# Optimization experiments

Measured on AMD Instinct MI355X. Metric: run time of the kernel, lower is better.

Reference implementation:

```python
import jax, jax.numpy as jnp
import numpy as np

B, T1, T2, V, D, H = 1024, 256, 256, 32004, 50, 64


def _lstm_scan(x, h0, c0, Wih, Whh, b):
    """PyTorch-gate-order LSTM over time. x: [B,T,D]; returns hs, cs: [B,T,H]."""
    def step(carry, xt):
        h, c = carry
        g = xt @ Wih.T + h @ Whh.T + b  # [B, 4H], gate order i,f,g,o
        i, f, gg, o = jnp.split(g, 4, axis=-1)
        c = jax.nn.sigmoid(f) * c + jax.nn.sigmoid(i) * jnp.tanh(gg)
        h = jax.nn.sigmoid(o) * jnp.tanh(c)
        return (h, c), (h, c)
    _, (hs, cs) = jax.lax.scan(step, (h0, c0), jnp.swapaxes(x, 0, 1))
    return jnp.swapaxes(hs, 0, 1), jnp.swapaxes(cs, 0, 1)


def setup_inputs() -> dict:
    key = jax.random.key(0)
    ks = jax.random.split(key, 20)
    s = 1.0 / np.sqrt(H).astype(np.float32)
    inp = {
        "sentence1": jax.random.randint(ks[0], (B, T1), 0, V),
        "sentence2": jax.random.randint(ks[1], (B, T2), 0, V),
        "s1_len": jax.random.randint(ks[2], (B, 1, H), 0, T1),
        "s2_len": jax.random.randint(ks[3], (B, 1, H), 0, T2),
        "s1_s": jax.random.randint(ks[4], (B,), 0, 2),
        "s2_s": jax.random.randint(ks[5], (B,), 0, 2),
        "emb": jax.random.normal(ks[6], (V, D), jnp.float32),
        "Wih1": jax.random.uniform(ks[7], (4 * H, D), jnp.float32, -s, s),
        "Whh1": jax.random.uniform(ks[8], (4 * H, H), jnp.float32, -s, s),
        "bih1": jax.random.uniform(ks[9], (4 * H,), jnp.float32, -s, s),
        "bhh1": jax.random.uniform(ks[10], (4 * H,), jnp.float32, -s, s),
        "Wih2": jax.random.uniform(ks[11], (4 * H, D), jnp.float32, -s, s),
        "Whh2": jax.random.uniform(ks[12], (4 * H, H), jnp.float32, -s, s),
        "bih2": jax.random.uniform(ks[13], (4 * H,), jnp.float32, -s, s),
        "bhh2": jax.random.uniform(ks[14], (4 * H,), jnp.float32, -s, s),
        "Wl1": jax.random.uniform(ks[15], (128, H), jnp.float32, -s, s),
        "bl1": jax.random.uniform(ks[16], (128,), jnp.float32, -s, s),
        "Wl2": jax.random.uniform(ks[17], (4, 128), jnp.float32, -0.1, 0.1),
        "bl2": jax.random.uniform(ks[18], (4,), jnp.float32, -0.1, 0.1),
    }
    return inp


def reference(sentence1, sentence2, s1_len, s2_len, s1_s, s2_s, emb,
              Wih1, Whh1, bih1, bhh1, Wih2, Whh2, bih2, bhh2, Wl1, bl1, Wl2, bl2):
    embed1 = emb[sentence1]  # [B,T1,D]
    embed2 = emb[sentence2]  # [B,T2,D]
    h0 = jnp.zeros((B, H), embed1.dtype)
    c0 = jnp.zeros((B, H), embed1.dtype)
    # manual LSTMCell loop in original == scanned LSTM, keep all h,c per step
    h, c = _lstm_scan(embed1, h0, c0, Wih1, Whh1, bih1 + bhh1)  # [B,T1,H]
    gather_h = jnp.take_along_axis(h, s1_len, axis=1)[:, 0, :]  # [B,H]
    gather_c = jnp.take_along_axis(c, s1_len, axis=1)[:, 0, :]
    out, _ = _lstm_scan(embed2, gather_h, gather_c, Wih2, Whh2, bih2 + bhh2)
    out = jnp.take_along_axis(out, s2_len, axis=1)[:, 0, :]  # [B,H]
    out = jnp.tanh(out @ Wl1.T + bl1)  # dropout is identity at inference
    out = out @ Wl2.T + bl2  # [B,4]
    return out
```

## Files before the change

kernel.cpp:

```cpp
#include <hip/hip_runtime.h>

#define Bsz 1024
#define Tt  256
#define Vv  32004
#define Dd  50
#define Hh  64
#define MB  128

typedef __bf16 b16x8 __attribute__((ext_vector_type(8)));
typedef float  f32x4 __attribute__((ext_vector_type(4)));

__device__ __forceinline__ void barrier_novm() {
    asm volatile("s_waitcnt lgkmcnt(0)\n\ts_barrier" ::: "memory");
}
__device__ __forceinline__ float fexp2(float x) {
    float r;
    asm("v_exp_f32 %0, %1" : "=v"(r) : "v"(x));
    return r;
}
__device__ __forceinline__ float frcp(float x) {
    float r;
    asm("v_rcp_f32 %0, %1" : "=v"(r) : "v"(x));
    return r;
}
__device__ __forceinline__ float fsig(float x) {
    return frcp(1.0f + fexp2(x * -1.442695041f));
}
__device__ __forceinline__ float ftanh(float x) {
    return 2.0f * frcp(1.0f + fexp2(x * -2.885390082f)) - 1.0f;
}

__device__ __forceinline__ void cvt_hilo(const float* x, b16x8& hi, b16x8& lo) {
#pragma unroll
    for (int e = 0; e < 8; ++e) {
        const __bf16 h = (__bf16)x[e];
        hi[e] = h;
        lo[e] = (__bf16)(x[e] - (float)h);
    }
}

__launch_bounds__(256)
__global__ void build_tables(const float* __restrict__ emb,
                             const float* __restrict__ Wih1,
                             const float* __restrict__ bih1,
                             const float* __restrict__ bhh1,
                             const float* __restrict__ Wih2,
                             const float* __restrict__ bih2,
                             const float* __restrict__ bhh2,
                             float* __restrict__ tab1,
                             float* __restrict__ tab2) {
    const int tid  = threadIdx.x;
    const int w    = tid >> 6;
    const int lane = tid & 63;
    const int q    = lane >> 4;
    const int mn   = lane & 15;
    const int v0   = blockIdx.x * MB;

    const float* Wih = blockIdx.y ? Wih2 : Wih1;
    const float* bih = blockIdx.y ? bih2 : bih1;
    const float* bhh = blockIdx.y ? bhh2 : bhh1;
    float*       tab = blockIdx.y ? tab2 : tab1;

    __shared__ __align__(16) float wlds[256 * Dd];
    __shared__ __align__(16) float elds[MB * Dd];

    for (int d4 = tid; d4 < 256 * Dd / 4; d4 += 256)
        *(float4*)&wlds[4 * d4] = *(const float4*)(Wih + 4 * d4);
    {
        const int ebase = v0 * Dd;
        const int elim  = Vv * Dd - ebase;
        const int mx    = Vv * Dd - 1;
        for (int d4 = tid; d4 < MB * Dd / 4; d4 += 256) {
            const int d = 4 * d4;
            float4 v;
            if (d + 4 <= elim) {
                v = *(const float4*)(emb + ebase + d);
            } else {
                v.x = emb[min(ebase + d,     mx)];
                v.y = emb[min(ebase + d + 1, mx)];
                v.z = emb[min(ebase + d + 2, mx)];
                v.w = emb[min(ebase + d + 3, mx)];
            }
            *(float4*)&elds[d] = v;
        }
    }
    __syncthreads();

    b16x8 bh[4][2], bl[4][2];
    f32x4 bias4;
#pragma unroll
    for (int k = 0; k < 4; ++k) {
        const int g = 64 * k + 16 * w + mn;
        const int base = g * Dd;
        float x[8];
#pragma unroll
        for (int j = 0; j < 8; ++j) x[j] = wlds[base + 8 * q + j];
        cvt_hilo(x, bh[k][0], bl[k][0]);
#pragma unroll
        for (int j = 0; j < 8; ++j) {
            const int col = 32 + 8 * q + j;
            x[j] = (col < Dd) ? wlds[base + col] : 0.0f;
        }
        cvt_hilo(x, bh[k][1], bl[k][1]);
        bias4[k] = bih[g] + bhh[g];
    }

#pragma unroll 1
    for (int m = 0; m < MB / 16; ++m) {
        const int base = (16 * m + mn) * Dd;
        b16x8 ah[2], al[2];
        float x[8];
#pragma unroll
        for (int j = 0; j < 8; ++j) x[j] = elds[base + 8 * q + j];
        cvt_hilo(x, ah[0], al[0]);
#pragma unroll
        for (int j = 0; j < 8; ++j) {
            const int col = 32 + 8 * q + j;
            x[j] = (col < Dd) ? elds[base + col] : 0.0f;
        }
        cvt_hilo(x, ah[1], al[1]);

        f32x4 acc[4];
#pragma unroll
        for (int k = 0; k < 4; ++k) {
            f32x4 a = {0.0f, 0.0f, 0.0f, 0.0f};
#pragma unroll
            for (int kh = 0; kh < 2; ++kh) {
                a = __builtin_amdgcn_mfma_f32_16x16x32_bf16(ah[kh], bh[k][kh], a, 0, 0, 0);
                a = __builtin_amdgcn_mfma_f32_16x16x32_bf16(ah[kh], bl[k][kh], a, 0, 0, 0);
                a = __builtin_amdgcn_mfma_f32_16x16x32_bf16(al[kh], bh[k][kh], a, 0, 0, 0);
            }
            acc[k] = a;
        }
#pragma unroll
        for (int r = 0; r < 4; ++r) {
            const int vr = v0 + 16 * m + 4 * q + r;
            if (vr < Vv) {
                f32x4 o;
                o[0] = acc[0][r] + bias4[0];
                o[1] = acc[1][r] + bias4[1];
                o[2] = acc[2][r] + bias4[2];
                o[3] = acc[3][r] + bias4[3];
                *(f32x4*)(tab + (size_t)vr * 256 + (16 * w + mn) * 4) = o;
            }
        }
    }
}

__launch_bounds__(256, 1)
__global__ void lstm_main(const int*   __restrict__ s1,
                          const int*   __restrict__ s2,
                          const int*   __restrict__ len1,
                          const int*   __restrict__ len2,
                          const float* __restrict__ tab1,
                          const float* __restrict__ tab2,
                          const float* __restrict__ Whh1,
                          const float* __restrict__ Whh2,
                          const float* __restrict__ Wl1,
                          const float* __restrict__ bl1,
                          const float* __restrict__ Wl2,
                          const float* __restrict__ bl2,
                          float* __restrict__ out) {
    const int tid  = threadIdx.x;
    const int w    = tid >> 6;
    const int lane = tid & 63;
    const int q    = lane >> 4;
    const int mn   = lane & 15;
    const int row  = mn & 3;
    const bool sb0 = (mn >> 2) & 1;
    const bool sb1 = (mn >> 3) & 1;
    const int u_own = 16 * w + 4 * q + (mn >> 2);
    const int b0   = blockIdx.x * 4;

    __shared__ __align__(16) __bf16 hsh[2][4][96];
    __shared__ int   toklds[Tt][4];
    __shared__ float h2s[4][64];
    __shared__ float ys[4][128];

    float c = 0.0f, selh = 0.0f, selc = 0.0f;
    const f32x4 zero4 = {0.0f, 0.0f, 0.0f, 0.0f};

    for (int phase = 0; phase < 2; ++phase) {
        const float* tab  = phase ? tab2 : tab1;
        const float* Whh  = phase ? Whh2 : Whh1;
        const int*   sent = phase ? s2 : s1;
        const int*   lenp = phase ? len2 : len1;

        for (int i = tid; i < 4 * Tt; i += 256)
            toklds[i & 255][i >> 8] = sent[(size_t)(b0 + (i >> 8)) * Tt + (i & 255)];

        b16x8 af[8];
#pragma unroll
        for (int k = 0; k < 4; ++k) {
            const int gate = 64 * k + 16 * w + mn;
#pragma unroll
            for (int kh = 0; kh < 2; ++kh) {
                const float* ar = Whh + (size_t)gate * Hh + kh * 32 + q * 8;
                const float4 f0 = *(const float4*)ar;
                const float4 f1 = *(const float4*)(ar + 4);
                b16x8 a;
                a[0] = (__bf16)f0.x; a[1] = (__bf16)f0.y;
                a[2] = (__bf16)f0.z; a[3] = (__bf16)f0.w;
                a[4] = (__bf16)f1.x; a[5] = (__bf16)f1.y;
                a[6] = (__bf16)f1.z; a[7] = (__bf16)f1.w;
                af[2 * k + kh] = a;
            }
        }

        const int mi = lenp[(size_t)(b0 + row) * Hh + u_own];

        const float h0f = phase ? selh : 0.0f;
        c = phase ? selc : 0.0f;
        hsh[0][row][u_own] = (__bf16)h0f;
        selh = 0.0f; selc = 0.0f;
        __syncthreads();

        const float* tu = tab + 4 * u_own;
        f32x4 Sa, Sb, Sc, Sd;
        auto prime = [&](int t, f32x4& S) {
            S = *(const f32x4*)(tu + (size_t)toklds[t][row] * 256);
        };
        prime(0, Sa); prime(1, Sb); prime(2, Sc); prime(3, Sd);

        auto pick = [&](const f32x4& a) -> float {
            const float e01 = sb0 ? a[1] : a[0];
            const float e23 = sb0 ? a[3] : a[2];
            return sb1 ? e23 : e01;
        };

        auto step = [&](int t, f32x4& S, int rb, int wb) {
            const b16x8 bf0 = *(const b16x8*)&hsh[rb][row][q * 8];
            const b16x8 bf1 = *(const b16x8*)&hsh[rb][row][32 + q * 8];
            const int tnext = (t + 4 < Tt) ? t + 4 : Tt - 1;
            const int tk = toklds[tnext][row];

            f32x4 aG = __builtin_amdgcn_mfma_f32_16x16x32_bf16(af[4], bf0, zero4, 0, 0, 0);
            aG = __builtin_amdgcn_mfma_f32_16x16x32_bf16(af[5], bf1, aG, 0, 0, 0);
            f32x4 aI = __builtin_amdgcn_mfma_f32_16x16x32_bf16(af[0], bf0, zero4, 0, 0, 0);
            aI = __builtin_amdgcn_mfma_f32_16x16x32_bf16(af[1], bf1, aI, 0, 0, 0);
            f32x4 aF = __builtin_amdgcn_mfma_f32_16x16x32_bf16(af[2], bf0, zero4, 0, 0, 0);
            aF = __builtin_amdgcn_mfma_f32_16x16x32_bf16(af[3], bf1, aF, 0, 0, 0);
            f32x4 aO = __builtin_amdgcn_mfma_f32_16x16x32_bf16(af[6], bf0, zero4, 0, 0, 0);
            aO = __builtin_amdgcn_mfma_f32_16x16x32_bf16(af[7], bf1, aO, 0, 0, 0);

            const float gG = pick(aG) + S[2];
            const float gI = pick(aI) + S[0];
            const float gF = pick(aF) + S[1];
            const float gO = pick(aO) + S[3];
            S = *(const f32x4*)(tu + (size_t)tk * 256);

            const float gv = ftanh(gG);
            const float iv = fsig(gI);
            const float fv = fsig(gF);
            const float ov = fsig(gO);
            c = fv * c + iv * gv;
            const float hv = ov * ftanh(c);
            hsh[wb][row][u_own] = (__bf16)hv;
            if (t == mi) { selh = hv; selc = c; }
            barrier_novm();
        };

        for (int t = 0; t < Tt; t += 4) {
            step(t,     Sa, 0, 1);
            step(t + 1, Sb, 1, 0);
            step(t + 2, Sc, 0, 1);
            step(t + 3, Sd, 1, 0);
        }
    }

    h2s[row][u_own] = selh;
    __syncthreads();
#pragma unroll
    for (int p = 0; p < 2; ++p) {
        const int idx = tid + 256 * p;
        const int rr = idx >> 7, n = idx & 127;
        float a = bl1[n];
        const float* wl = Wl1 + n * 64;
#pragma unroll 8
        for (int k = 0; k < 64; ++k) a += h2s[rr][k] * wl[k];
        ys[rr][n] = ftanh(a);
    }
    __syncthreads();
    if (tid < 16) {
        const int rr = tid >> 2, o = tid & 3;
        float a = bl2[o];
        const float* wl = Wl2 + o * 128;
#pragma unroll 8
        for (int k = 0; k < 128; ++k) a += ys[rr][k] * wl[k];
        out[(size_t)(b0 + rr) * 4 + o] = a;
    }
}

extern "C" void kernel_launch(void* const* d_in, const int* in_sizes, int n_in,
                              void* d_out, int out_size, void* d_ws, size_t ws_size,
                              hipStream_t stream) {
    const int*   s1   = (const int*)d_in[0];
    const int*   s2   = (const int*)d_in[1];
    const int*   l1   = (const int*)d_in[2];
    const int*   l2   = (const int*)d_in[3];
    const float* emb  = (const float*)d_in[6];
    const float* Wih1 = (const float*)d_in[7];
    const float* Whh1 = (const float*)d_in[8];
    const float* bih1 = (const float*)d_in[9];
    const float* bhh1 = (const float*)d_in[10];
    const float* Wih2 = (const float*)d_in[11];
    const float* Whh2 = (const float*)d_in[12];
    const float* bih2 = (const float*)d_in[13];
    const float* bhh2 = (const float*)d_in[14];
    const float* Wl1  = (const float*)d_in[15];
    const float* bl1  = (const float*)d_in[16];
    const float* Wl2  = (const float*)d_in[17];
    const float* bl2  = (const float*)d_in[18];
    float* out = (float*)d_out;

    float* tab1 = (float*)d_ws;
    float* tab2 = tab1 + (size_t)Vv * 256;

    dim3 grid((Vv + MB - 1) / MB, 2);
    build_tables<<<grid, 256, 0, stream>>>(emb, Wih1, bih1, bhh1,
                                           Wih2, bih2, bhh2, tab1, tab2);
    lstm_main<<<Bsz / 4, 256, 0, stream>>>(s1, s2, l1, l2, tab1, tab2,
                                           Whh1, Whh2, Wl1, bl1, Wl2, bl2, out);
}
```

Before: 281.5 us.

## Process two batch-row groups per block and fold activation scales into weights

Each block now handles 8 batch rows, interleaving two independent LSTM recurrences per thread to hide MFMA and transcendental latency per serial step. Gate prescale constants for exp2-based sigmoid/tanh are folded into the precomputed input table and the recurrent weights, removing multiplies from the step. Tokens are stored row-major in LDS and fetched as int4 vectors with deeper table prefetch. The grid halves, leaving fewer blocks than CUs, and per-thread register pressure rises.

```diff
diff --git a/kernel.cpp b/kernel.cpp
--- a/kernel.cpp
+++ b/kernel.cpp
@@ -23,9 +23,8 @@
     asm("v_rcp_f32 %0, %1" : "=v"(r) : "v"(x));
     return r;
 }
-__device__ __forceinline__ float fsig(float x) {
-    return frcp(1.0f + fexp2(x * -1.442695041f));
-}
+__device__ __forceinline__ float fsig_p(float x)  { return frcp(1.0f + fexp2(x)); }
+__device__ __forceinline__ float ftanh_p(float x) { return 2.0f * frcp(1.0f + fexp2(x)) - 1.0f; }
 __device__ __forceinline__ float ftanh(float x) {
     return 2.0f * frcp(1.0f + fexp2(x * -2.885390082f)) - 1.0f;
 }
@@ -105,6 +104,8 @@
         bias4[k] = bih[g] + bhh[g];
     }
 
+    const f32x4 scale4 = {-1.442695041f, -1.442695041f, -2.885390082f, -1.442695041f};
+
 #pragma unroll 1
     for (int m = 0; m < MB / 16; ++m) {
         const int base = (16 * m + mn) * Dd;
@@ -137,10 +138,10 @@
             const int vr = v0 + 16 * m + 4 * q + r;
             if (vr < Vv) {
                 f32x4 o;
-                o[0] = acc[0][r] + bias4[0];
-                o[1] = acc[1][r] + bias4[1];
-                o[2] = acc[2][r] + bias4[2];
-                o[3] = acc[3][r] + bias4[3];
+                o[0] = (acc[0][r] + bias4[0]) * scale4[0];
+                o[1] = (acc[1][r] + bias4[1]) * scale4[1];
+                o[2] = (acc[2][r] + bias4[2]) * scale4[2];
+                o[3] = (acc[3][r] + bias4[3]) * scale4[3];
                 *(f32x4*)(tab + (size_t)vr * 256 + (16 * w + mn) * 4) = o;
             }
         }
@@ -166,18 +167,20 @@
     const int lane = tid & 63;
     const int q    = lane >> 4;
     const int mn   = lane & 15;
-    const int row  = mn & 3;
+    const int rowA = mn & 3;
+    const int rowB = rowA + 4;
     const bool sb0 = (mn >> 2) & 1;
     const bool sb1 = (mn >> 3) & 1;
     const int u_own = 16 * w + 4 * q + (mn >> 2);
-    const int b0   = blockIdx.x * 4;
-
-    __shared__ __align__(16) __bf16 hsh[2][4][96];
-    __shared__ int   toklds[Tt][4];
-    __shared__ float h2s[4][64];
-    __shared__ float ys[4][128];
-
-    float c = 0.0f, selh = 0.0f, selc = 0.0f;
+    const int b0   = blockIdx.x * 8;
+
+    __shared__ __align__(16) __bf16 hsh[2][8][96];
+    __shared__ __align__(16) int toklds[8][Tt + 8];
+    __shared__ float h2s[8][64];
+    __shared__ float ys[8][128];
+
+    float cA = 0.0f, selhA = 0.0f, selcA = 0.0f;
+    float cB = 0.0f, selhB = 0.0f, selcB = 0.0f;
     const f32x4 zero4 = {0.0f, 0.0f, 0.0f, 0.0f};
 
     for (int phase = 0; phase < 2; ++phase) {
@@ -186,41 +189,57 @@
         const int*   sent = phase ? s2 : s1;
         const int*   lenp = phase ? len2 : len1;
 
-        for (int i = tid; i < 4 * Tt; i += 256)
-            toklds[i & 255][i >> 8] = sent[(size_t)(b0 + (i >> 8)) * Tt + (i & 255)];
+        for (int i = tid; i < 8 * Tt; i += 256)
+            toklds[i >> 8][i & 255] = sent[(size_t)(b0 + (i >> 8)) * Tt + (i & 255)];
 
         b16x8 af[8];
 #pragma unroll
         for (int k = 0; k < 4; ++k) {
             const int gate = 64 * k + 16 * w + mn;
+            const float sck = (k == 2) ? -2.885390082f : -1.442695041f;
 #pragma unroll
             for (int kh = 0; kh < 2; ++kh) {
                 const float* ar = Whh + (size_t)gate * Hh + kh * 32 + q * 8;
                 const float4 f0 = *(const float4*)ar;
                 const float4 f1 = *(const float4*)(ar + 4);
                 b16x8 a;
-                a[0] = (__bf16)f0.x; a[1] = (__bf16)f0.y;
-                a[2] = (__bf16)f0.z; a[3] = (__bf16)f0.w;
-                a[4] = (__bf16)f1.x; a[5] = (__bf16)f1.y;
-                a[6] = (__bf16)f1.z; a[7] = (__bf16)f1.w;
+                a[0] = (__bf16)(f0.x * sck); a[1] = (__bf16)(f0.y * sck);
+                a[2] = (__bf16)(f0.z * sck); a[3] = (__bf16)(f0.w * sck);
+                a[4] = (__bf16)(f1.x * sck); a[5] = (__bf16)(f1.y * sck);
+                a[6] = (__bf16)(f1.z * sck); a[7] = (__bf16)(f1.w * sck);
                 af[2 * k + kh] = a;
             }
         }
 
-        const int mi = lenp[(size_t)(b0 + row) * Hh + u_own];
-
-        const float h0f = phase ? selh : 0.0f;
-        c = phase ? selc : 0.0f;
-        hsh[0][row][u_own] = (__bf16)h0f;
-        selh = 0.0f; selc = 0.0f;
+        const int miA = lenp[(size_t)(b0 + rowA) * Hh + u_own];
+        const int miB = lenp[(size_t)(b0 + rowB) * Hh + u_own];
+
+        hsh[0][rowA][u_own] = (__bf16)(phase ? selhA : 0.0f);
+        hsh[0][rowB][u_own] = (__bf16)(phase ? selhB : 0.0f);
+        cA = phase ? selcA : 0.0f;
+        cB = phase ? selcB : 0.0f;
+        selhA = 0.0f; selcA = 0.0f; selhB = 0.0f; selcB = 0.0f;
         __syncthreads();
 
         const float* tu = tab + 4 * u_own;
-        f32x4 Sa, Sb, Sc, Sd;
-        auto prime = [&](int t, f32x4& S) {
-            S = *(const f32x4*)(tu + (size_t)toklds[t][row] * 256);
-        };
-        prime(0, Sa); prime(1, Sb); prime(2, Sc); prime(3, Sd);
+
+        int4 a0c = *(const int4*)&toklds[rowA][0];
+        int4 aC1 = *(const int4*)&toklds[rowA][4];
+        int4 aC2 = *(const int4*)&toklds[rowA][8];
+        int4 b0c = *(const int4*)&toklds[rowB][0];
+        int4 bC1 = *(const int4*)&toklds[rowB][4];
+        int4 bC2 = *(const int4*)&toklds[rowB][8];
+
+        f32x4 SA0, SA1, SA2, SA3, SA4, SA5, SA6, SA7;
+        f32x4 SB0, SB1, SB2, SB3, SB4, SB5, SB6, SB7;
+        SA0 = *(const f32x4*)(tu + (size_t)a0c.x * 256);
+        SA1 = *(const f32x4*)(tu + (size_t)a0c.y * 256);
+        SA2 = *(const f32x4*)(tu + (size_t)a0c.z * 256);
+        SA3 = *(const f32x4*)(tu + (size_t)a0c.w * 256);
+        SB0 = *(const f32x4*)(tu + (size_t)b0c.x * 256);
+        SB1 = *(const f32x4*)(tu + (size_t)b0c.y * 256);
+        SB2 = *(const f32x4*)(tu + (size_t)b0c.z * 256);
+        SB3 = *(const f32x4*)(tu + (size_t)b0c.w * 256);
 
         auto pick = [&](const f32x4& a) -> float {
             const float e01 = sb0 ? a[1] : a[0];
@@ -228,60 +247,100 @@
             return sb1 ? e23 : e01;
         };
 
-        auto step = [&](int t, f32x4& S, int rb, int wb) {
-            const b16x8 bf0 = *(const b16x8*)&hsh[rb][row][q * 8];
-            const b16x8 bf1 = *(const b16x8*)&hsh[rb][row][32 + q * 8];
-            const int tnext = (t + 4 < Tt) ? t + 4 : Tt - 1;
-            const int tk = toklds[tnext][row];
-
-            f32x4 aG = __builtin_amdgcn_mfma_f32_16x16x32_bf16(af[4], bf0, zero4, 0, 0, 0);
-            aG = __builtin_amdgcn_mfma_f32_16x16x32_bf16(af[5], bf1, aG, 0, 0, 0);
-            f32x4 aI = __builtin_amdgcn_mfma_f32_16x16x32_bf16(af[0], bf0, zero4, 0, 0, 0);
-            aI = __builtin_amdgcn_mfma_f32_16x16x32_bf16(af[1], bf1, aI, 0, 0, 0);
-            f32x4 aF = __builtin_amdgcn_mfma_f32_16x16x32_bf16(af[2], bf0, zero4, 0, 0, 0);
-            aF = __builtin_amdgcn_mfma_f32_16x16x32_bf16(af[3], bf1, aF, 0, 0, 0);
-            f32x4 aO = __builtin_amdgcn_mfma_f32_16x16x32_bf16(af[6], bf0, zero4, 0, 0, 0);
-            aO = __builtin_amdgcn_mfma_f32_16x16x32_bf16(af[7], bf1, aO, 0, 0, 0);
-
-            const float gG = pick(aG) + S[2];
-            const float gI = pick(aI) + S[0];
-            const float gF = pick(aF) + S[1];
-            const float gO = pick(aO) + S[3];
-            S = *(const f32x4*)(tu + (size_t)tk * 256);
-
-            const float gv = ftanh(gG);
-            const float iv = fsig(gI);
-            const float fv = fsig(gF);
-            const float ov = fsig(gO);
-            c = fv * c + iv * gv;
-            const float hv = ov * ftanh(c);
-            hsh[wb][row][u_own] = (__bf16)hv;
-            if (t == mi) { selh = hv; selc = c; }
+        auto sstep = [&](int i, f32x4& SuA, f32x4& SfA, int tokA,
+                                f32x4& SuB, f32x4& SfB, int tokB, int tb) {
+            SfA = *(const f32x4*)(tu + (size_t)tokA * 256);
+            SfB = *(const f32x4*)(tu + (size_t)tokB * 256);
+
+            const int rb = i & 1, wb = rb ^ 1;
+            const b16x8 bA0 = *(const b16x8*)&hsh[rb][rowA][q * 8];
+            const b16x8 bA1 = *(const b16x8*)&hsh[rb][rowA][32 + q * 8];
+            const b16x8 bB0 = *(const b16x8*)&hsh[rb][rowB][q * 8];
+            const b16x8 bB1 = *(const b16x8*)&hsh[rb][rowB][32 + q * 8];
+
+            f32x4 aGA = __builtin_amdgcn_mfma_f32_16x16x32_bf16(af[4], bA0, zero4, 0, 0, 0);
+            aGA = __builtin_amdgcn_mfma_f32_16x16x32_bf16(af[5], bA1, aGA, 0, 0, 0);
+            f32x4 aIA = __builtin_amdgcn_mfma_f32_16x16x32_bf16(af[0], bA0, zero4, 0, 0, 0);
+            aIA = __builtin_amdgcn_mfma_f32_16x16x32_bf16(af[1], bA1, aIA, 0, 0, 0);
+            f32x4 aFA = __builtin_amdgcn_mfma_f32_16x16x32_bf16(af[2], bA0, zero4, 0, 0, 0);
+            aFA = __builtin_amdgcn_mfma_f32_16x16x32_bf16(af[3], bA1, aFA, 0, 0, 0);
+            f32x4 aOA = __builtin_amdgcn_mfma_f32_16x16x32_bf16(af[6], bA0, zero4, 0, 0, 0);
+            aOA = __builtin_amdgcn_mfma_f32_16x16x32_bf16(af[7], bA1, aOA, 0, 0, 0);
+
+            f32x4 aGB = __builtin_amdgcn_mfma_f32_16x16x32_bf16(af[4], bB0, zero4, 0, 0, 0);
+            aGB = __builtin_amdgcn_mfma_f32_16x16x32_bf16(af[5], bB1, aGB, 0, 0, 0);
+            f32x4 aIB = __builtin_amdgcn_mfma_f32_16x16x32_bf16(af[0], bB0, zero4, 0, 0, 0);
+            aIB = __builtin_amdgcn_mfma_f32_16x16x32_bf16(af[1], bB1, aIB, 0, 0, 0);
+            f32x4 aFB = __builtin_amdgcn_mfma_f32_16x16x32_bf16(af[2], bB0, zero4, 0, 0, 0);
+            aFB = __builtin_amdgcn_mfma_f32_16x16x32_bf16(af[3], bB1, aFB, 0, 0, 0);
+            f32x4 aOB = __builtin_amdgcn_mfma_f32_16x16x32_bf16(af[6], bB0, zero4, 0, 0, 0);
+            aOB = __builtin_amdgcn_mfma_f32_16x16x32_bf16(af[7], bB1, aOB, 0, 0, 0);
+
+            {
+                const float gG = pick(aGA) + SuA[2];
+                const float gI = pick(aIA) + SuA[0];
+                const float gF = pick(aFA) + SuA[1];
+                const float gO = pick(aOA) + SuA[3];
+                const float gv = ftanh_p(gG);
+                const float iv = fsig_p(gI);
+                const float fv = fsig_p(gF);
+                const float ov = fsig_p(gO);
+                cA = fv * cA + iv * gv;
+                const float hv = ov * ftanh(cA);
+                hsh[wb][rowA][u_own] = (__bf16)hv;
+                if (tb + i == miA) { selhA = hv; selcA = cA; }
+            }
+            {
+                const float gG = pick(aGB) + SuB[2];
+                const float gI = pick(aIB) + SuB[0];
+                const float gF = pick(aFB) + SuB[1];
+                const float gO = pick(aOB) + SuB[3];
+                const float gv = ftanh_p(gG);
+                const float iv = fsig_p(gI);
+                const float fv = fsig_p(gF);
+                const float ov = fsig_p(gO);
+                cB = fv * cB + iv * gv;
+                const float hv = ov * ftanh(cB);
+                hsh[wb][rowB][u_own] = (__bf16)hv;
+                if (tb + i == miB) { selhB = hv; selcB = cB; }
+            }
             barrier_novm();
         };
 
-        for (int t = 0; t < Tt; t += 4) {
-            step(t,     Sa, 0, 1);
-            step(t + 1, Sb, 1, 0);
-            step(t + 2, Sc, 0, 1);
-            step(t + 3, Sd, 1, 0);
-        }
-    }
-
-    h2s[row][u_own] = selh;
+        for (int tb = 0; tb < Tt; tb += 8) {
+            sstep(0, SA0, SA4, aC1.x, SB0, SB4, bC1.x, tb);
+            sstep(1, SA1, SA5, aC1.y, SB1, SB5, bC1.y, tb);
+            const int nb1 = min(tb + 12, Tt - 4);
+            const int4 aN1 = *(const int4*)&toklds[rowA][nb1];
+            const int4 bN1 = *(const int4*)&toklds[rowB][nb1];
+            sstep(2, SA2, SA6, aC1.z, SB2, SB6, bC1.z, tb);
+            const int nb2 = min(tb + 16, Tt - 4);
+            const int4 aN2 = *(const int4*)&toklds[rowA][nb2];
+            const int4 bN2 = *(const int4*)&toklds[rowB][nb2];
+            sstep(3, SA3, SA7, aC1.w, SB3, SB7, bC1.w, tb);
+            sstep(4, SA4, SA0, aC2.x, SB4, SB0, bC2.x, tb);
+            sstep(5, SA5, SA1, aC2.y, SB5, SB1, bC2.y, tb);
+            sstep(6, SA6, SA2, aC2.z, SB6, SB2, bC2.z, tb);
+            sstep(7, SA7, SA3, aC2.w, SB7, SB3, bC2.w, tb);
+            aC1 = aN1; aC2 = aN2; bC1 = bN1; bC2 = bN2;
+        }
+    }
+
+    h2s[rowA][u_own] = selhA;
+    h2s[rowB][u_own] = selhB;
     __syncthreads();
 #pragma unroll
-    for (int p = 0; p < 2; ++p) {
+    for (int p = 0; p < 4; ++p) {
         const int idx = tid + 256 * p;
         const int rr = idx >> 7, n = idx & 127;
         float a = bl1[n];
         const float* wl = Wl1 + n * 64;
 #pragma unroll 8
         for (int k = 0; k < 64; ++k) a += h2s[rr][k] * wl[k];
-        ys[rr][n] = ftanh(a);
+        ys[rr][n] = ftanh(a * -0.346573590f * -2.885390082f);
     }
     __syncthreads();
-    if (tid < 16) {
+    if (tid < 32) {
         const int rr = tid >> 2, o = tid & 3;
         float a = bl2[o];
         const float* wl = Wl2 + o * 128;
@@ -319,6 +378,6 @@
     dim3 grid((Vv + MB - 1) / MB, 2);
     build_tables<<<grid, 256, 0, stream>>>(emb, Wih1, bih1, bhh1,
                                            Wih2, bih2, bhh2, tab1, tab2);
-    lstm_main<<<Bsz / 4, 256, 0, stream>>>(s1, s2, l1, l2, tab1, tab2,
+    lstm_main<<<Bsz / 8, 256, 0, stream>>>(s1, s2, l1, l2, tab1, tab2,
                                            Whh1, Whh2, Wl1, bl1, Wl2, bl2, out);
 }
```

After: 361.3 us. 28.3% more time.
